# Optimization experiments

Measured on AMD Instinct MI355X. Metric: run time of the kernel, lower is better.

## Reference

```python
import jax, jax.numpy as jnp
import numpy as np

D_MODEL = 768
NUM_HEADS = 12
DEPTH = D_MODEL // NUM_HEADS


def setup_inputs() -> dict:
    key = jax.random.key(0)
    ks = jax.random.split(key, 11)
    B, S, D = 2, 2048, D_MODEL
    scale = 1.0 / np.sqrt(D)
    inp = {
        "v": jax.random.normal(ks[0], (B, S, D), jnp.float32),
        "k": jax.random.normal(ks[1], (B, S, D), jnp.float32),
        "q": jax.random.normal(ks[2], (B, S, D), jnp.float32),
        "wq": jax.random.normal(ks[3], (D, D), jnp.float32) * scale,
        "bq": jnp.zeros((D,), jnp.float32),
        "wk": jax.random.normal(ks[4], (D, D), jnp.float32) * scale,
        "bk": jnp.zeros((D,), jnp.float32),
        "wv": jax.random.normal(ks[5], (D, D), jnp.float32) * scale,
        "bv": jnp.zeros((D,), jnp.float32),
        "wo": jax.random.normal(ks[6], (D, D), jnp.float32) * scale,
        "bo": jnp.zeros((D,), jnp.float32),
    }
    return inp


def _split_heads(x):
    # (B, S, D) -> (B, H, S, depth)
    B, S, _ = x.shape
    return x.reshape(B, S, NUM_HEADS, DEPTH).transpose(0, 2, 1, 3)


def reference(v, k, q, wq, bq, wk, bk, wv, bv, wo, bo):
    B, S, D = q.shape
    qh = _split_heads(q @ wq + bq)  # (B,H,S,dh)
    kh = _split_heads(k @ wk + bk)
    vh = _split_heads(v @ wv + bv)
    logits = jnp.einsum("bhqd,bhkd->bhqk", qh, kh) / jnp.sqrt(
        jnp.asarray(DEPTH, qh.dtype)
    )
    attn = jax.nn.softmax(logits, axis=-1)  # (B,H,S,S)
    ctx = jnp.einsum("bhqk,bhkd->bhqd", attn, vh)
    ctx = ctx.transpose(0, 2, 1, 3).reshape(B, S, D)
    return ctx @ wo + bo
```

## Files before the change

### kernel.cpp

```cpp
#include <hip/hip_runtime.h>
#include <hip/hip_bf16.h>
#include <math.h>

typedef __bf16 bf16;
typedef __attribute__((ext_vector_type(8))) __bf16 bf16x8;
typedef __attribute__((ext_vector_type(4))) __bf16 bf16x4v;
typedef __attribute__((ext_vector_type(4))) float f32x4;

#define MFMA16(a, b, c) __builtin_amdgcn_mfma_f32_16x16x32_bf16(a, b, c, 0, 0, 0)

__device__ __forceinline__ void gld16(const bf16* g, bf16* l) {
  __builtin_amdgcn_global_load_lds((const __attribute__((address_space(1))) void*)g,
                                   (__attribute__((address_space(3))) void*)l, 16, 0, 0);
}

__global__ __launch_bounds__(256) void prep(const float* __restrict__ q,
                                            const float* __restrict__ k,
                                            const float* __restrict__ v,
                                            bf16* __restrict__ qb, bf16* __restrict__ kb,
                                            bf16* __restrict__ vb,
                                            const float* __restrict__ w0,
                                            const float* __restrict__ w1,
                                            const float* __restrict__ w2,
                                            const float* __restrict__ w3,
                                            bf16* __restrict__ t0, bf16* __restrict__ t1,
                                            bf16* __restrict__ t2, bf16* __restrict__ t3) {
  const int lin = blockIdx.x;
  if (lin < 4608) {
    const int which = lin / 1536, idx = lin % 1536;
    const float* a = which == 0 ? q : (which == 1 ? k : v);
    bf16* o = which == 0 ? qb : (which == 1 ? kb : vb);
    const size_t i = ((size_t)idx * 256 + threadIdx.x) * 8;
    const float4 f0 = *(const float4*)(a + i);
    const float4 f1 = *(const float4*)(a + i + 4);
    bf16x8 r = {(bf16)f0.x, (bf16)f0.y, (bf16)f0.z, (bf16)f0.w,
                (bf16)f1.x, (bf16)f1.y, (bf16)f1.z, (bf16)f1.w};
    *(bf16x8*)(o + i) = r;
  } else {
    const int w = lin - 4608;
    const int z = w / 576, rem = w % 576;
    const int by = rem / 24, bx = rem % 24;
    const float* W = z == 0 ? w0 : (z == 1 ? w1 : (z == 2 ? w2 : w3));
    bf16* T = z == 0 ? t0 : (z == 1 ? t1 : (z == 2 ? t2 : t3));
    __shared__ float t[32][33];
    const int tx = threadIdx.x & 31, ty = threadIdx.x >> 5;
    const int c0 = bx * 32, r0 = by * 32;
#pragma unroll
    for (int i = 0; i < 4; ++i) {
      const int r = ty + 8 * i;
      t[r][tx] = W[(size_t)(r0 + r) * 768 + c0 + tx];
    }
    __syncthreads();
#pragma unroll
    for (int i = 0; i < 4; ++i) {
      const int r = ty + 8 * i;
      T[(size_t)(c0 + r) * 768 + r0 + tx] = (bf16)t[tx][r];
    }
  }
}

__device__ __forceinline__ void gemm_core(const bf16* __restrict__ A, const bf16* __restrict__ BT,
                                          int row0, int col0, bf16* As, bf16* Bs,
                                          f32x4 acc[4][4]) {
  const int tid = threadIdx.x;
  const int lane = tid & 63, wave = tid >> 6;
  const int m15 = lane & 15, kg = lane >> 4;
  const int wm = wave >> 1, wn = wave & 1;
  const int pr16 = lane & 15;
  const int pk8 = (lane >> 4) * 8;
#pragma unroll
  for (int i = 0; i < 4; ++i)
#pragma unroll
    for (int j = 0; j < 4; ++j) acc[i][j] = f32x4{0.f, 0.f, 0.f, 0.f};

  for (int k0 = 0; k0 < 768; k0 += 32) {
#pragma unroll
    for (int j = 0; j < 2; ++j) {
      const int i = wave * 2 + j;
      gld16(A + (size_t)(row0 + 16 * i + pr16) * 768 + k0 + pk8, As + i * 512);
      gld16(BT + (size_t)(col0 + 16 * i + pr16) * 768 + k0 + pk8, Bs + i * 512);
    }
    __syncthreads();
    bf16x8 af[4], bfr[4];
#pragma unroll
    for (int t = 0; t < 4; ++t)
      af[t] = *(const bf16x8*)(As + (4 * wm + t) * 512 + kg * 128 + m15 * 8);
#pragma unroll
    for (int t = 0; t < 4; ++t)
      bfr[t] = *(const bf16x8*)(Bs + (4 * wn + t) * 512 + kg * 128 + m15 * 8);
#pragma unroll
    for (int mt = 0; mt < 4; ++mt)
#pragma unroll
      for (int nt = 0; nt < 4; ++nt) acc[mt][nt] = MFMA16(af[mt], bfr[nt], acc[mt][nt]);
    __syncthreads();
  }
}

__global__ __launch_bounds__(256, 3) void gemm_qkv(
    const bf16* __restrict__ qb, const bf16* __restrict__ kb, const bf16* __restrict__ vb,
    const bf16* __restrict__ wqT, const bf16* __restrict__ wkT, const bf16* __restrict__ wvT,
    const float* __restrict__ bq, const float* __restrict__ bk, const float* __restrict__ bv,
    bf16* __restrict__ Qh, bf16* __restrict__ Kh, bf16* __restrict__ Vt) {
  __shared__ bf16 As[128 * 32], Bs[128 * 32];
  const bf16 *A, *BT;
  const float* bias;
  bf16* out;
  int mode;
  if (blockIdx.z == 0) { A = qb; BT = wqT; bias = bq; out = Qh; mode = 0; }
  else if (blockIdx.z == 1) { A = kb; BT = wkT; bias = bk; out = Kh; mode = 0; }
  else { A = vb; BT = wvT; bias = bv; out = Vt; mode = 1; }
  const int row0 = blockIdx.y * 128, col0 = blockIdx.x * 128;
  f32x4 acc[4][4];
  gemm_core(A, BT, row0, col0, As, Bs, acc);

  const int lane = threadIdx.x & 63, wave = threadIdx.x >> 6;
  const int m15 = lane & 15, kg = lane >> 4;
  const int wm = wave >> 1, wn = wave & 1;
#pragma unroll
  for (int mt = 0; mt < 4; ++mt) {
#pragma unroll
    for (int nt = 0; nt < 4; ++nt) {
      const int col = col0 + 64 * wn + 16 * nt + m15;
      const float bb = bias[col];
      const int h = col >> 6, d = col & 63;
      const int rowb = row0 + 64 * wm + 16 * mt + kg * 4;
      const int b = rowb >> 11, s0 = rowb & 2047;
      if (mode == 0) {
#pragma unroll
        for (int r = 0; r < 4; ++r)
          out[((size_t)(b * 12 + h) * 2048 + s0 + r) * 64 + d] = (bf16)(acc[mt][nt][r] + bb);
      } else {
        bf16x4v pk;
#pragma unroll
        for (int r = 0; r < 4; ++r) pk[r] = (bf16)(acc[mt][nt][r] + bb);
        *(bf16x4v*)&out[((size_t)(b * 12 + h) * 64 + d) * 2048 + s0] = pk;
      }
    }
  }
}

__global__ __launch_bounds__(256, 3) void gemm_out(const bf16* __restrict__ A,
                                                   const bf16* __restrict__ BT,
                                                   const float* __restrict__ bias,
                                                   float* __restrict__ out) {
  __shared__ bf16 As[64 * 32], Bs[64 * 32];
  const int tid = threadIdx.x;
  const int lane = tid & 63, wave = tid >> 6;
  const int m15 = lane & 15, kg = lane >> 4;
  const int wm = wave >> 1, wn = wave & 1;
  const int row0 = blockIdx.y * 64, col0 = blockIdx.x * 64;
  const int pr16 = lane & 15, pk8 = (lane >> 4) * 8;

  f32x4 acc[2][2];
#pragma unroll
  for (int i = 0; i < 2; ++i)
#pragma unroll
    for (int j = 0; j < 2; ++j) acc[i][j] = f32x4{0.f, 0.f, 0.f, 0.f};

  for (int k0 = 0; k0 < 768; k0 += 32) {
    gld16(A + (size_t)(row0 + 16 * wave + pr16) * 768 + k0 + pk8, As + wave * 512);
    gld16(BT + (size_t)(col0 + 16 * wave + pr16) * 768 + k0 + pk8, Bs + wave * 512);
    __syncthreads();
    bf16x8 af[2], bfr[2];
#pragma unroll
    for (int t = 0; t < 2; ++t)
      af[t] = *(const bf16x8*)(As + (2 * wm + t) * 512 + kg * 128 + m15 * 8);
#pragma unroll
    for (int t = 0; t < 2; ++t)
      bfr[t] = *(const bf16x8*)(Bs + (2 * wn + t) * 512 + kg * 128 + m15 * 8);
#pragma unroll
    for (int mt = 0; mt < 2; ++mt)
#pragma unroll
      for (int nt = 0; nt < 2; ++nt) acc[mt][nt] = MFMA16(af[mt], bfr[nt], acc[mt][nt]);
    __syncthreads();
  }
#pragma unroll
  for (int mt = 0; mt < 2; ++mt) {
#pragma unroll
    for (int nt = 0; nt < 2; ++nt) {
      const int col = col0 + 32 * wn + 16 * nt + m15;
      const float bb = bias[col];
#pragma unroll
      for (int r = 0; r < 4; ++r) {
        const int row = row0 + 32 * wm + 16 * mt + kg * 4 + r;
        out[(size_t)row * 768 + col] = acc[mt][nt][r] + bb;
      }
    }
  }
}

__global__ __launch_bounds__(128, 2) void attn_kernel(const bf16* __restrict__ Q,
                                                      const bf16* __restrict__ K,
                                                      const bf16* __restrict__ VT,
                                                      bf16* __restrict__ ctx) {
  __shared__ bf16 Ks[2][4096];
  __shared__ bf16 Vs[2][4096];
  __shared__ bf16 P[2][2][16 * 68];

  const int tid = threadIdx.x;
  const int lane = tid & 63, wave = tid >> 6;
  const int m15 = lane & 15, kg = lane >> 4;
  const int lin = blockIdx.x;
  const int bh = lin % 24, qb_ = lin / 24;
  const size_t hb = (size_t)bh * 2048 * 64;
  const bf16* Qp = Q + hb;
  const bf16* Kp = K + hb;
  const bf16* Vp = VT + hb;
  const int qrow0 = qb_ * 64 + wave * 32;

  const int pr = lane & 7;
  const int pc = (lane >> 3) * 8;

  bf16x8 qf[2][2];
#pragma unroll
  for (int t = 0; t < 2; ++t)
#pragma unroll
    for (int ks = 0; ks < 2; ++ks) {
      bf16x8 tv = *(const bf16x8*)&Qp[(size_t)(qrow0 + 16 * t + m15) * 64 + 32 * ks + kg * 8];
#pragma unroll
      for (int j = 0; j < 8; ++j) tv[j] = (bf16)((float)tv[j] * 0.125f);
      qf[t][ks] = tv;
    }

  f32x4 o0[4], o1[4];
  float lp0[4], lp1[4];
#pragma unroll
  for (int nt = 0; nt < 4; ++nt) { o0[nt] = f32x4{0.f, 0.f, 0.f, 0.f}; o1[nt] = f32x4{0.f, 0.f, 0.f, 0.f}; }
#pragma unroll
  for (int r = 0; r < 4; ++r) { lp0[r] = 0.f; lp1[r] = 0.f; }

#pragma unroll
  for (int j = 0; j < 4; ++j) {
    const int i = wave * 4 + j;
    gld16(Kp + (size_t)(8 * i + pr) * 64 + pc, &Ks[0][i * 512]);
    gld16(Vp + (size_t)(8 * i + pr) * 2048 + pc, &Vs[0][i * 512]);
  }

  for (int c = 0; c < 32; ++c) {
    const int buf = c & 1;
    const int kc = c * 64;
    __syncthreads();
    if (c < 31) {
      const int nb = buf ^ 1, nkc = kc + 64;
#pragma unroll
      for (int j = 0; j < 4; ++j) {
        const int i = wave * 4 + j;
        gld16(Kp + (size_t)(nkc + 8 * i + pr) * 64 + pc, &Ks[nb][i * 512]);
        gld16(Vp + (size_t)(8 * i + pr) * 2048 + nkc + pc, &Vs[nb][i * 512]);
      }
    }
    f32x4 s0[4], s1[4];
#pragma unroll
    for (int nt = 0; nt < 4; ++nt) { s0[nt] = f32x4{0.f, 0.f, 0.f, 0.f}; s1[nt] = f32x4{0.f, 0.f, 0.f, 0.f}; }
#pragma unroll
    for (int ks = 0; ks < 2; ++ks) {
#pragma unroll
      for (int nt = 0; nt < 4; ++nt) {
        const int key = 16 * nt + m15;
        const bf16x8 kf =
            *(const bf16x8*)&Ks[buf][(key >> 3) * 512 + (4 * ks + kg) * 64 + (key & 7) * 8];
        s0[nt] = MFMA16(qf[0][ks], kf, s0[nt]);
        s1[nt] = MFMA16(qf[1][ks], kf, s1[nt]);
      }
    }
#pragma unroll
    for (int r = 0; r < 4; ++r) {
#pragma unroll
      for (int nt = 0; nt < 4; ++nt) {
        const float p0 = __expf(s0[nt][r]);
        const float p1 = __expf(s1[nt][r]);
        lp0[r] += p0;
        lp1[r] += p1;
        P[wave][0][(kg * 4 + r) * 68 + 16 * nt + m15] = (bf16)p0;
        P[wave][1][(kg * 4 + r) * 68 + 16 * nt + m15] = (bf16)p1;
      }
    }
    asm volatile("s_waitcnt lgkmcnt(0)" ::: "memory");
#pragma unroll
    for (int ks = 0; ks < 2; ++ks) {
      const bf16x8 pf0 = *(const bf16x8*)&P[wave][0][m15 * 68 + 32 * ks + kg * 8];
      const bf16x8 pf1 = *(const bf16x8*)&P[wave][1][m15 * 68 + 32 * ks + kg * 8];
#pragma unroll
      for (int nt = 0; nt < 4; ++nt) {
        const int d = 16 * nt + m15;
        const bf16x8 vf =
            *(const bf16x8*)&Vs[buf][(d >> 3) * 512 + (4 * ks + kg) * 64 + (d & 7) * 8];
        o0[nt] = MFMA16(pf0, vf, o0[nt]);
        o1[nt] = MFMA16(pf1, vf, o1[nt]);
      }
    }
  }

#pragma unroll
  for (int r = 0; r < 4; ++r) {
#pragma unroll
    for (int st = 1; st < 16; st <<= 1) {
      lp0[r] += __shfl_xor(lp0[r], st);
      lp1[r] += __shfl_xor(lp1[r], st);
    }
  }

  const int b = bh / 12, h = bh % 12;
#pragma unroll
  for (int nt = 0; nt < 4; ++nt) {
#pragma unroll
    for (int r = 0; r < 4; ++r) {
      const int sr0 = qrow0 + kg * 4 + r;
      ctx[((size_t)(b * 2048) + sr0) * 768 + h * 64 + 16 * nt + m15] = (bf16)(o0[nt][r] / lp0[r]);
      ctx[((size_t)(b * 2048) + sr0 + 16) * 768 + h * 64 + 16 * nt + m15] = (bf16)(o1[nt][r] / lp1[r]);
    }
  }
}

extern "C" void kernel_launch(void* const* d_in, const int* in_sizes, int n_in,
                              void* d_out, int out_size, void* d_ws, size_t ws_size,
                              hipStream_t stream) {
  const float* v = (const float*)d_in[0];
  const float* k = (const float*)d_in[1];
  const float* q = (const float*)d_in[2];
  const float* wq = (const float*)d_in[3];
  const float* bq = (const float*)d_in[4];
  const float* wk = (const float*)d_in[5];
  const float* bk = (const float*)d_in[6];
  const float* wv = (const float*)d_in[7];
  const float* bv = (const float*)d_in[8];
  const float* wo = (const float*)d_in[9];
  const float* bo = (const float*)d_in[10];

  char* ws = (char*)d_ws;
  const size_t SEG = (size_t)4096 * 768 * sizeof(bf16);
  const size_t WSEG = (size_t)768 * 768 * sizeof(bf16);
  bf16* Qh = (bf16*)(ws + 0 * SEG);
  bf16* Kh = (bf16*)(ws + 1 * SEG);
  bf16* Vt = (bf16*)(ws + 2 * SEG);
  bf16* qb = (bf16*)(ws + 3 * SEG);
  bf16* kb = (bf16*)(ws + 4 * SEG);
  bf16* vb = (bf16*)(ws + 5 * SEG);
  bf16* ctx = qb;
  bf16* wqT = (bf16*)(ws + 6 * SEG);
  bf16* wkT = (bf16*)(ws + 6 * SEG + WSEG);
  bf16* wvT = (bf16*)(ws + 6 * SEG + 2 * WSEG);
  bf16* woT = (bf16*)(ws + 6 * SEG + 3 * WSEG);

  prep<<<dim3(6912), 256, 0, stream>>>(q, k, v, qb, kb, vb, wq, wk, wv, wo,
                                       wqT, wkT, wvT, woT);
  gemm_qkv<<<dim3(6, 32, 3), 256, 0, stream>>>(qb, kb, vb, wqT, wkT, wvT, bq, bk, bv,
                                               Qh, Kh, Vt);
  attn_kernel<<<dim3(768), 128, 0, stream>>>(Qh, Kh, Vt, ctx);
  gemm_out<<<dim3(12, 64), 256, 0, stream>>>(ctx, woT, bo, (float*)d_out);
}
```

Baseline: 227.0 us.

## Split attention key range across two wave pairs and merge partial outputs

The attention block grows from 2 to 4 waves. Each pair of waves processes half of the key sequence in 32-key chunks using its own double-buffered K/V region in a unified shared buffer. At the end, the partial accumulators and row sums are combined through shared memory before normalization. This intra-block split-K is meant to raise the number of waves in flight and hide latency, at the cost of more LDS, an extra reduction step and smaller MFMA work per chunk.

```diff
diff --git a/kernel.cpp b/kernel.cpp
--- a/kernel.cpp
+++ b/kernel.cpp
@@ -189,27 +189,27 @@
   }
 }
 
-__global__ __launch_bounds__(128, 2) void attn_kernel(const bf16* __restrict__ Q,
+__global__ __launch_bounds__(256, 3) void attn_kernel(const bf16* __restrict__ Q,
                                                       const bf16* __restrict__ K,
                                                       const bf16* __restrict__ VT,
                                                       bf16* __restrict__ ctx) {
-  __shared__ bf16 Ks[2][4096];
-  __shared__ bf16 Vs[2][4096];
-  __shared__ bf16 P[2][2][16 * 68];
+  __shared__ __align__(16) bf16 S[21504];
 
   const int tid = threadIdx.x;
   const int lane = tid & 63, wave = tid >> 6;
   const int m15 = lane & 15, kg = lane >> 4;
   const int lin = blockIdx.x;
-  const int bh = lin % 24, qb_ = lin / 24;
+  const int bh = lin % 24, qblk = lin / 24;
   const size_t hb = (size_t)bh * 2048 * 64;
   const bf16* Qp = Q + hb;
   const bf16* Kp = K + hb;
   const bf16* Vp = VT + hb;
-  const int qrow0 = qb_ * 64 + wave * 32;
-
-  const int pr = lane & 7;
-  const int pc = (lane >> 3) * 8;
+  const int pipe = wave >> 1;
+  const int qrow0 = qblk * 64 + (wave & 1) * 32;
+  bf16* Pw = S + 16384 + wave * 1280;
+
+  const int kpr = lane & 7, kpc = (lane >> 3) * 8;
+  const int vpr = lane & 15, vpc = (lane >> 4) * 8;
 
   bf16x8 qf[2][2];
 #pragma unroll
@@ -222,93 +222,138 @@
       qf[t][ks] = tv;
     }
 
-  f32x4 o0[4], o1[4];
-  float lp0[4], lp1[4];
-#pragma unroll
-  for (int nt = 0; nt < 4; ++nt) { o0[nt] = f32x4{0.f, 0.f, 0.f, 0.f}; o1[nt] = f32x4{0.f, 0.f, 0.f, 0.f}; }
-#pragma unroll
-  for (int r = 0; r < 4; ++r) { lp0[r] = 0.f; lp1[r] = 0.f; }
+  f32x4 o[2][4];
+  float lp[2][4];
+#pragma unroll
+  for (int t = 0; t < 2; ++t) {
+#pragma unroll
+    for (int nt = 0; nt < 4; ++nt) o[t][nt] = f32x4{0.f, 0.f, 0.f, 0.f};
+#pragma unroll
+    for (int r = 0; r < 4; ++r) lp[t][r] = 0.f;
+  }
 
 #pragma unroll
   for (int j = 0; j < 4; ++j) {
-    const int i = wave * 4 + j;
-    gld16(Kp + (size_t)(8 * i + pr) * 64 + pc, &Ks[0][i * 512]);
-    gld16(Vp + (size_t)(8 * i + pr) * 2048 + pc, &Vs[0][i * 512]);
+    const int idx = wave * 4 + j;
+    const int sp = idx >> 3, r8 = idx & 7;
+    const int kc = sp * 1024;
+    if (r8 < 4)
+      gld16(Kp + (size_t)(kc + 8 * r8 + kpr) * 64 + kpc, S + sp * 2 * 2048 + r8 * 512);
+    else {
+      const int i = r8 - 4;
+      gld16(Vp + (size_t)(16 * i + vpr) * 2048 + kc + vpc, S + 8192 + sp * 2 * 2048 + i * 512);
+    }
   }
 
   for (int c = 0; c < 32; ++c) {
     const int buf = c & 1;
-    const int kc = c * 64;
     __syncthreads();
     if (c < 31) {
-      const int nb = buf ^ 1, nkc = kc + 64;
+      const int nb = buf ^ 1;
 #pragma unroll
       for (int j = 0; j < 4; ++j) {
-        const int i = wave * 4 + j;
-        gld16(Kp + (size_t)(nkc + 8 * i + pr) * 64 + pc, &Ks[nb][i * 512]);
-        gld16(Vp + (size_t)(8 * i + pr) * 2048 + nkc + pc, &Vs[nb][i * 512]);
-      }
-    }
-    f32x4 s0[4], s1[4];
-#pragma unroll
-    for (int nt = 0; nt < 4; ++nt) { s0[nt] = f32x4{0.f, 0.f, 0.f, 0.f}; s1[nt] = f32x4{0.f, 0.f, 0.f, 0.f}; }
+        const int idx = wave * 4 + j;
+        const int sp = idx >> 3, r8 = idx & 7;
+        const int kc = sp * 1024 + (c + 1) * 32;
+        if (r8 < 4)
+          gld16(Kp + (size_t)(kc + 8 * r8 + kpr) * 64 + kpc,
+                S + (sp * 2 + nb) * 2048 + r8 * 512);
+        else {
+          const int i = r8 - 4;
+          gld16(Vp + (size_t)(16 * i + vpr) * 2048 + kc + vpc,
+                S + 8192 + (sp * 2 + nb) * 2048 + i * 512);
+        }
+      }
+    }
+    const bf16* KsB = S + (pipe * 2 + buf) * 2048;
+    const bf16* VsB = S + 8192 + (pipe * 2 + buf) * 2048;
+
+    f32x4 s[2][2];
+#pragma unroll
+    for (int t = 0; t < 2; ++t)
+#pragma unroll
+      for (int nt = 0; nt < 2; ++nt) s[t][nt] = f32x4{0.f, 0.f, 0.f, 0.f};
 #pragma unroll
     for (int ks = 0; ks < 2; ++ks) {
 #pragma unroll
-      for (int nt = 0; nt < 4; ++nt) {
+      for (int nt = 0; nt < 2; ++nt) {
         const int key = 16 * nt + m15;
         const bf16x8 kf =
-            *(const bf16x8*)&Ks[buf][(key >> 3) * 512 + (4 * ks + kg) * 64 + (key & 7) * 8];
-        s0[nt] = MFMA16(qf[0][ks], kf, s0[nt]);
-        s1[nt] = MFMA16(qf[1][ks], kf, s1[nt]);
-      }
-    }
-#pragma unroll
-    for (int r = 0; r < 4; ++r) {
+            *(const bf16x8*)&KsB[(key >> 3) * 512 + (4 * ks + kg) * 64 + (key & 7) * 8];
+        s[0][nt] = MFMA16(qf[0][ks], kf, s[0][nt]);
+        s[1][nt] = MFMA16(qf[1][ks], kf, s[1][nt]);
+      }
+    }
+#pragma unroll
+    for (int t = 0; t < 2; ++t)
+#pragma unroll
+      for (int r = 0; r < 4; ++r)
+#pragma unroll
+        for (int nt = 0; nt < 2; ++nt) {
+          const float pe = __expf(s[t][nt][r]);
+          lp[t][r] += pe;
+          Pw[t * 640 + (kg * 4 + r) * 40 + 16 * nt + m15] = (bf16)pe;
+        }
+    asm volatile("s_waitcnt lgkmcnt(0)" ::: "memory");
+    const bf16x8 pf0 = *(const bf16x8*)&Pw[0 * 640 + m15 * 40 + kg * 8];
+    const bf16x8 pf1 = *(const bf16x8*)&Pw[1 * 640 + m15 * 40 + kg * 8];
+#pragma unroll
+    for (int nt = 0; nt < 4; ++nt) {
+      const int d = 16 * nt + m15;
+      const bf16x8 vf =
+          *(const bf16x8*)&VsB[(d >> 4) * 512 + kg * 128 + (d & 15) * 8];
+      o[0][nt] = MFMA16(pf0, vf, o[0][nt]);
+      o[1][nt] = MFMA16(pf1, vf, o[1][nt]);
+    }
+  }
+
+  __syncthreads();
+  float* sc = (float*)S;
+  if (wave >= 2) {
+    const int rg = (wave - 2) * 2560;
+#pragma unroll
+    for (int t = 0; t < 2; ++t)
+#pragma unroll
+      for (int nt = 0; nt < 4; ++nt)
+        *(f32x4*)&sc[rg + (t * 4 + nt) * 256 + lane * 4] = o[t][nt];
+    f32x4 l0 = {lp[0][0], lp[0][1], lp[0][2], lp[0][3]};
+    f32x4 l1 = {lp[1][0], lp[1][1], lp[1][2], lp[1][3]};
+    *(f32x4*)&sc[rg + 2048 + lane * 8] = l0;
+    *(f32x4*)&sc[rg + 2048 + lane * 8 + 4] = l1;
+  }
+  __syncthreads();
+  if (wave < 2) {
+    const int rg = wave * 2560;
+#pragma unroll
+    for (int t = 0; t < 2; ++t)
 #pragma unroll
       for (int nt = 0; nt < 4; ++nt) {
-        const float p0 = __expf(s0[nt][r]);
-        const float p1 = __expf(s1[nt][r]);
-        lp0[r] += p0;
-        lp1[r] += p1;
-        P[wave][0][(kg * 4 + r) * 68 + 16 * nt + m15] = (bf16)p0;
-        P[wave][1][(kg * 4 + r) * 68 + 16 * nt + m15] = (bf16)p1;
-      }
-    }
-    asm volatile("s_waitcnt lgkmcnt(0)" ::: "memory");
-#pragma unroll
-    for (int ks = 0; ks < 2; ++ks) {
-      const bf16x8 pf0 = *(const bf16x8*)&P[wave][0][m15 * 68 + 32 * ks + kg * 8];
-      const bf16x8 pf1 = *(const bf16x8*)&P[wave][1][m15 * 68 + 32 * ks + kg * 8];
-#pragma unroll
-      for (int nt = 0; nt < 4; ++nt) {
-        const int d = 16 * nt + m15;
-        const bf16x8 vf =
-            *(const bf16x8*)&Vs[buf][(d >> 3) * 512 + (4 * ks + kg) * 64 + (d & 7) * 8];
-        o0[nt] = MFMA16(pf0, vf, o0[nt]);
-        o1[nt] = MFMA16(pf1, vf, o1[nt]);
-      }
-    }
-  }
-
-#pragma unroll
-  for (int r = 0; r < 4; ++r) {
-#pragma unroll
-    for (int st = 1; st < 16; st <<= 1) {
-      lp0[r] += __shfl_xor(lp0[r], st);
-      lp1[r] += __shfl_xor(lp1[r], st);
-    }
-  }
-
-  const int b = bh / 12, h = bh % 12;
-#pragma unroll
-  for (int nt = 0; nt < 4; ++nt) {
-#pragma unroll
-    for (int r = 0; r < 4; ++r) {
-      const int sr0 = qrow0 + kg * 4 + r;
-      ctx[((size_t)(b * 2048) + sr0) * 768 + h * 64 + 16 * nt + m15] = (bf16)(o0[nt][r] / lp0[r]);
-      ctx[((size_t)(b * 2048) + sr0 + 16) * 768 + h * 64 + 16 * nt + m15] = (bf16)(o1[nt][r] / lp1[r]);
-    }
+        const f32x4 po = *(const f32x4*)&sc[rg + (t * 4 + nt) * 256 + lane * 4];
+#pragma unroll
+        for (int j = 0; j < 4; ++j) o[t][nt][j] += po[j];
+      }
+    const f32x4 pl0 = *(const f32x4*)&sc[rg + 2048 + lane * 8];
+    const f32x4 pl1 = *(const f32x4*)&sc[rg + 2048 + lane * 8 + 4];
+#pragma unroll
+    for (int r = 0; r < 4; ++r) { lp[0][r] += pl0[r]; lp[1][r] += pl1[r]; }
+#pragma unroll
+    for (int t = 0; t < 2; ++t)
+#pragma unroll
+      for (int r = 0; r < 4; ++r) {
+#pragma unroll
+        for (int st = 1; st < 16; st <<= 1) lp[t][r] += __shfl_xor(lp[t][r], st);
+      }
+    const int b = bh / 12, h = bh % 12;
+#pragma unroll
+    for (int t = 0; t < 2; ++t)
+#pragma unroll
+      for (int nt = 0; nt < 4; ++nt)
+#pragma unroll
+        for (int r = 0; r < 4; ++r) {
+          const int sr = qrow0 + 16 * t + kg * 4 + r;
+          ctx[((size_t)(b * 2048) + sr) * 768 + h * 64 + 16 * nt + m15] =
+              (bf16)(o[t][nt][r] / lp[t][r]);
+        }
   }
 }
 
@@ -346,6 +391,6 @@
                                        wqT, wkT, wvT, woT);
   gemm_qkv<<<dim3(6, 32, 3), 256, 0, stream>>>(qb, kb, vb, wqT, wkT, wvT, bq, bk, bv,
                                                Qh, Kh, Vt);
-  attn_kernel<<<dim3(768), 128, 0, stream>>>(Qh, Kh, Vt, ctx);
+  attn_kernel<<<dim3(768), 256, 0, stream>>>(Qh, Kh, Vt, ctx);
   gemm_out<<<dim3(12, 64), 256, 0, stream>>>(ctx, woT, bo, (float*)d_out);
 }
```

After: 214.2 us. 1.06x faster.
